# Performance work log

Measured on AMD Instinct MI355X. Metric: run time of the kernel, lower is better.

Reference implementation:

```python
import jax, jax.numpy as jnp
import numpy as np

B, N, M, D, F, H = 8, 512, 512, 512, 512, 8
D_H, F_H = D // H, F // H


def setup_inputs() -> dict:
    key = jax.random.key(0)
    ks = jax.random.split(key, 7)
    X = jax.random.normal(ks[0], (B, N, D), dtype=jnp.float32)
    V = jax.random.normal(ks[1], (B, M, F), dtype=jnp.float32)
    # learned parameters, init normal(0, 0.02) as in the torch module
    W_Q_1 = 0.02 * jax.random.normal(ks[2], (H, N, D_H, D_H), dtype=jnp.float32)
    W_Q_2 = 0.02 * jax.random.normal(ks[3], (H, N, M, D_H), dtype=jnp.float32)
    W_V = 0.02 * jax.random.normal(ks[4], (H, F_H, F_H), dtype=jnp.float32)
    O_w = 0.02 * jax.random.normal(ks[5], (F, F), dtype=jnp.float32)
    O_b = jnp.zeros((F,), dtype=jnp.float32)
    return {"X": X, "V": V, "W_Q_1": W_Q_1, "W_Q_2": W_Q_2,
            "W_V": W_V, "O_w": O_w, "O_b": O_b}


def reference(X, V, W_Q_1, W_Q_2, W_V, O_w, O_b):
    b, n, d = X.shape
    _, m, f = V.shape
    Xh = X.reshape(b, n, H, d // H)      # [B,N,H,D_H]
    Vh = V.reshape(b, m, H, f // H)      # [B,M,H,F_H]
    # 'hndd' repeats d within one operand -> diagonal of W_Q_1's last two dims
    # (faithful to torch.einsum semantics): per-position per-channel scale.
    Q_1 = jnp.einsum('bnhd,hndd->bhnd', Xh, W_Q_1)
    Q_1 = jax.nn.gelu(Q_1, approximate=False)  # torch nn.GELU default = exact erf
    Q_2 = jnp.einsum('bhnd,hnmd->bhnm', Q_1, W_Q_2)  # synthesized attention logits
    A = jax.nn.softmax(Q_2, axis=3)                  # softmax over M
    # 'hff' likewise takes the diagonal of W_V -> per-head channel scale fused
    # with the attention-weighted value aggregation.
    Y = jnp.einsum('bhnm,bmhf,hff->bnhf', A, Vh, W_V)
    Y = Y.reshape(b, n, f)
    return Y @ O_w.T + O_b
```

## Files before the change

### kernel.cpp

```cpp
#include <hip/hip_runtime.h>
#include <cstdint>

#define B_ 8
#define N_ 512
#define M_ 512
#define D_ 512
#define F_ 512
#define H_ 8
#define DH_ 64
#define FH_ 64

typedef __attribute__((ext_vector_type(8))) short bf16x8;
typedef __attribute__((ext_vector_type(4))) float f32x4;
typedef __attribute__((ext_vector_type(8))) unsigned short u16x8;

__device__ __forceinline__ unsigned short f2bf(float x) {
    unsigned u = __float_as_uint(x);
    return (unsigned short)((u + 0x7fffu + ((u >> 16) & 1u)) >> 16);
}
__device__ __forceinline__ float bf2f(unsigned short b) {
    return __uint_as_float(((unsigned)b) << 16);
}

__device__ __forceinline__ f32x4 ntload4(const float* p) {
    return __builtin_nontemporal_load((const f32x4*)p);
}
__device__ __forceinline__ float ntload1(const float* p) {
    return __builtin_nontemporal_load(p);
}

template <int CTRL>
__device__ __forceinline__ float dpp_add(float x) {
    int y = __builtin_amdgcn_update_dpp(0, __float_as_int(x), CTRL, 0xf, 0xf, true);
    return x + __int_as_float(y);
}

__global__ __launch_bounds__(256, 4) void syn_k_attn(const float* __restrict__ X,
                                                     const float* __restrict__ W1,
                                                     const float* __restrict__ W2,
                                                     unsigned short* __restrict__ Ahi,
                                                     unsigned short* __restrict__ Alo) {
    int hn = blockIdx.x;
    int h = hn >> 9, n = hn & 511;
    int t = threadIdx.x;
    int wave = t >> 6, lane = t & 63;
    __shared__ float q1s[8 * 68];
    __shared__ float logits[8 * 520];

    {
        int d = t & 63;
        int b0 = t >> 6;
        float w = ntload1(W1 + (size_t)hn * (DH_ * DH_) + d * (DH_ + 1));
        #pragma unroll
        for (int i = 0; i < 2; ++i) {
            int bi = b0 + i * 4;
            float x = X[((size_t)(bi * N_ + n)) * D_ + h * DH_ + d];
            float v = x * w;
            q1s[bi * 68 + d] = 0.5f * v * (1.0f + erff(v * 0.70710678118654752440f));
        }
    }
    __syncthreads();

    int mr = lane >> 3, c = lane & 7;
    float4 qa[8], qb[8];
    #pragma unroll
    for (int b = 0; b < 8; ++b) {
        qa[b] = *(const float4*)&q1s[b * 68 + c * 8];
        qb[b] = *(const float4*)&q1s[b * 68 + c * 8 + 4];
    }

    const float* w2 = W2 + (size_t)hn * ((size_t)M_ * DH_);
    #pragma unroll 4
    for (int g = 0; g < 16; ++g) {
        int m = (wave + g * 4) * 8 + mr;
        const float* wr = w2 + (size_t)m * DH_ + c * 8;
        f32x4 wa = ntload4(wr);
        f32x4 wb = ntload4(wr + 4);
        float acc[8];
        #pragma unroll
        for (int b = 0; b < 8; ++b) {
            float a0 = wa.x * qa[b].x + wa.y * qa[b].y + wa.z * qa[b].z + wa.w * qa[b].w
                     + wb.x * qb[b].x + wb.y * qb[b].y + wb.z * qb[b].z + wb.w * qb[b].w;
            a0 = dpp_add<0xB1>(a0);
            a0 = dpp_add<0x4E>(a0);
            a0 = dpp_add<0x124>(a0);
            acc[b] = a0;
        }
        float lo = c == 0 ? acc[0] : c == 1 ? acc[1] : c == 2 ? acc[2] : acc[3];
        float hi = c == 0 ? acc[4] : c == 1 ? acc[5] : c == 2 ? acc[6] : acc[7];
        if (c < 4) {
            logits[c * 520 + m] = lo;
            logits[(c + 4) * 520 + m] = hi;
        }
    }
    __syncthreads();

    for (int bb = wave; bb < 8; bb += 4) {
        const float* lrow = &logits[bb * 520 + lane * 8];
        float4 va = *(const float4*)lrow;
        float4 vb = *(const float4*)(lrow + 4);
        float v[8] = {va.x, va.y, va.z, va.w, vb.x, vb.y, vb.z, vb.w};
        float mx = v[0];
        #pragma unroll
        for (int i = 1; i < 8; ++i) mx = fmaxf(mx, v[i]);
        #pragma unroll
        for (int s = 1; s < 64; s <<= 1) mx = fmaxf(mx, __shfl_xor(mx, s));
        float e[8]; float sum = 0.f;
        #pragma unroll
        for (int i = 0; i < 8; ++i) { e[i] = expf(v[i] - mx); sum += e[i]; }
        #pragma unroll
        for (int s = 1; s < 64; s <<= 1) sum += __shfl_xor(sum, s);
        float inv = 1.0f / sum;
        unsigned short hb[8], lb[8];
        #pragma unroll
        for (int i = 0; i < 8; ++i) {
            float y = e[i] * inv;
            hb[i] = f2bf(y);
            lb[i] = f2bf(y - bf2f(hb[i]));
        }
        size_t base = ((size_t)(bb * H_ + h) * N_ + n) * M_ + lane * 8;
        *(u16x8*)(Ahi + base) = *(u16x8*)hb;
        *(u16x8*)(Alo + base) = *(u16x8*)lb;
    }
}

__global__ __launch_bounds__(256) void syn_k_splitw(const float* __restrict__ Ow,
                                                    unsigned short* __restrict__ Whi,
                                                    unsigned short* __restrict__ Wlo) {
    int i = (blockIdx.x * 256 + threadIdx.x) * 4;
    float4 v = *(const float4*)(Ow + i);
    float vv[4] = {v.x, v.y, v.z, v.w};
    unsigned short hb[4], lb[4];
    #pragma unroll
    for (int j = 0; j < 4; ++j) {
        hb[j] = f2bf(vv[j]);
        lb[j] = f2bf(vv[j] - bf2f(hb[j]));
    }
    uint2 hv, lv;
    hv.x = (unsigned)hb[0] | ((unsigned)hb[1] << 16);
    hv.y = (unsigned)hb[2] | ((unsigned)hb[3] << 16);
    lv.x = (unsigned)lb[0] | ((unsigned)lb[1] << 16);
    lv.y = (unsigned)lb[2] | ((unsigned)lb[3] << 16);
    *(uint2*)(Whi + i) = hv;
    *(uint2*)(Wlo + i) = lv;
}

__global__ __launch_bounds__(256) void syn_k_splitv(const float* __restrict__ V,
                                                    unsigned short* __restrict__ Vthi,
                                                    unsigned short* __restrict__ Vtlo) {
    int bh = blockIdx.x;
    int b = bh >> 3, h = bh & 7;
    int t = threadIdx.x;
    __shared__ float lds[64 * 68];
    for (int m0 = 0; m0 < M_; m0 += 64) {
        int m = t >> 2, fo = (t & 3) * 16;
        const float* src = V + ((size_t)(b * M_ + m0 + m)) * F_ + h * FH_ + fo;
        #pragma unroll
        for (int i = 0; i < 4; ++i)
            *(float4*)&lds[m * 68 + fo + i * 4] = *(const float4*)(src + i * 4);
        __syncthreads();
        int f = t >> 2, mo = (t & 3) * 16;
        unsigned short hb[16], lb[16];
        #pragma unroll
        for (int i = 0; i < 16; ++i) {
            float x = lds[(mo + i) * 68 + f];
            hb[i] = f2bf(x);
            lb[i] = f2bf(x - bf2f(hb[i]));
        }
        size_t base = ((size_t)(bh * 64 + f)) * 512 + m0 + mo;
        *(u16x8*)(Vthi + base) = *(u16x8*)hb;
        *(u16x8*)(Vthi + base + 8) = *(u16x8*)&hb[8];
        *(u16x8*)(Vtlo + base) = *(u16x8*)lb;
        *(u16x8*)(Vtlo + base + 8) = *(u16x8*)&lb[8];
        __syncthreads();
    }
}

__global__ __launch_bounds__(256) void syn_k_pv_mfma(const unsigned short* __restrict__ Ahi,
                                                     const unsigned short* __restrict__ Alo,
                                                     const unsigned short* __restrict__ Vthi,
                                                     const unsigned short* __restrict__ Vtlo,
                                                     const float* __restrict__ WV,
                                                     unsigned short* __restrict__ Yhi,
                                                     unsigned short* __restrict__ Ylo) {
    int bh = blockIdx.y;
    int b = bh >> 3, h = bh & 7;
    int n0 = blockIdx.x * 32;
    int t = threadIdx.x;
    int lane = t & 63, wave = t >> 6;
    int wr = wave >> 1, wc = wave & 1;
    __shared__ __align__(16) unsigned short Alh[32 * 64], All[32 * 64];
    __shared__ __align__(16) unsigned short Blh[64 * 64], Bll[64 * 64];
    f32x4 acc[2];
    acc[0] = (f32x4){0.f, 0.f, 0.f, 0.f};
    acc[1] = (f32x4){0.f, 0.f, 0.f, 0.f};

    int srow = t >> 3, skg = t & 7;
    int sslot = skg ^ (srow & 7);
    const unsigned short* Ahb = Ahi + ((size_t)bh * N_ + n0) * M_;
    const unsigned short* Alb = Alo + ((size_t)bh * N_ + n0) * M_;
    const unsigned short* Vhb = Vthi + ((size_t)bh * 64) * 512;
    const unsigned short* Vlb = Vtlo + ((size_t)bh * 64) * 512;

    u16x8 rAh, rAl, rBh0, rBl0, rBh1, rBl1;
    {
        size_t aoff = (size_t)srow * M_ + skg * 8;
        rAh = *(const u16x8*)(Ahb + aoff);
        rAl = *(const u16x8*)(Alb + aoff);
        size_t v0 = (size_t)srow * 512 + skg * 8;
        size_t v1 = (size_t)(srow + 32) * 512 + skg * 8;
        rBh0 = *(const u16x8*)(Vhb + v0);
        rBl0 = *(const u16x8*)(Vlb + v0);
        rBh1 = *(const u16x8*)(Vhb + v1);
        rBl1 = *(const u16x8*)(Vlb + v1);
    }

    #pragma unroll 1
    for (int mb = 0; mb < 8; ++mb) {
        *(u16x8*)&Alh[srow * 64 + sslot * 8] = rAh;
        *(u16x8*)&All[srow * 64 + sslot * 8] = rAl;
        *(u16x8*)&Blh[srow * 64 + sslot * 8] = rBh0;
        *(u16x8*)&Bll[srow * 64 + sslot * 8] = rBl0;
        *(u16x8*)&Blh[(srow + 32) * 64 + sslot * 8] = rBh1;
        *(u16x8*)&Bll[(srow + 32) * 64 + sslot * 8] = rBl1;
        __syncthreads();
        if (mb < 7) {
            int m0 = (mb + 1) * 64;
            size_t aoff = (size_t)srow * M_ + m0 + skg * 8;
            rAh = *(const u16x8*)(Ahb + aoff);
            rAl = *(const u16x8*)(Alb + aoff);
            size_t v0 = (size_t)srow * 512 + m0 + skg * 8;
            size_t v1 = (size_t)(srow + 32) * 512 + m0 + skg * 8;
            rBh0 = *(const u16x8*)(Vhb + v0);
            rBl0 = *(const u16x8*)(Vlb + v0);
            rBh1 = *(const u16x8*)(Vhb + v1);
            rBl1 = *(const u16x8*)(Vlb + v1);
        }
        #pragma unroll
        for (int mg = 0; mg < 2; ++mg) {
            int kslot = (mg * 4 + (lane >> 4)) ^ (lane & 7);
            int arow = wr * 16 + (lane & 15);
            bf16x8 afh = *(const bf16x8*)&Alh[arow * 64 + kslot * 8];
            bf16x8 afl = *(const bf16x8*)&All[arow * 64 + kslot * 8];
            bf16x8 bfh[2], bfl[2];
            #pragma unroll
            for (int j = 0; j < 2; ++j) {
                int brow = wc * 32 + j * 16 + (lane & 15);
                bfh[j] = *(const bf16x8*)&Blh[brow * 64 + kslot * 8];
                bfl[j] = *(const bf16x8*)&Bll[brow * 64 + kslot * 8];
            }
            #pragma unroll
            for (int j = 0; j < 2; ++j) {
                acc[j] = __builtin_amdgcn_mfma_f32_16x16x32_bf16(afh, bfh[j], acc[j], 0, 0, 0);
                acc[j] = __builtin_amdgcn_mfma_f32_16x16x32_bf16(afh, bfl[j], acc[j], 0, 0, 0);
                acc[j] = __builtin_amdgcn_mfma_f32_16x16x32_bf16(afl, bfh[j], acc[j], 0, 0, 0);
            }
        }
        __syncthreads();
    }

    int crow = n0 + wr * 16 + (lane >> 4) * 4;
    int ccol = wc * 32 + (lane & 15);
    #pragma unroll
    for (int j = 0; j < 2; ++j) {
        int f = ccol + j * 16;
        float s = WV[(size_t)h * (FH_ * FH_) + f * (FH_ + 1)];
        #pragma unroll
        for (int r = 0; r < 4; ++r) {
            int row = crow + r;
            float y = acc[j][r] * s;
            unsigned short hb = f2bf(y);
            unsigned short lb = f2bf(y - bf2f(hb));
            size_t base = ((size_t)(b * N_ + row)) * F_ + h * FH_ + f;
            Yhi[base] = hb;
            Ylo[base] = lb;
        }
    }
}

__global__ __launch_bounds__(256) void syn_k_out_mfma(const unsigned short* __restrict__ Yhi,
                                                      const unsigned short* __restrict__ Ylo,
                                                      const unsigned short* __restrict__ Whi,
                                                      const unsigned short* __restrict__ Wlo,
                                                      const float* __restrict__ Ob,
                                                      float* __restrict__ out) {
    int r0 = blockIdx.x * 64;
    int f0 = blockIdx.y * 64;
    int t = threadIdx.x;
    int lane = t & 63, wave = t >> 6;
    int wr = wave >> 1, wc = wave & 1;
    __shared__ __align__(16) unsigned short Alh[64 * 64], All[64 * 64];
    __shared__ __align__(16) unsigned short Blh[64 * 64], Bll[64 * 64];
    f32x4 acc[2][2];
    #pragma unroll
    for (int i = 0; i < 2; ++i)
        #pragma unroll
        for (int j = 0; j < 2; ++j) acc[i][j] = (f32x4){0.f, 0.f, 0.f, 0.f};

    int srow = t >> 3, skg = t & 7;
    int sslot = skg ^ (srow & 7);

    #pragma unroll 1
    for (int kb = 0; kb < 512; kb += 64) {
        #pragma unroll
        for (int rr = 0; rr < 2; ++rr) {
            int row = srow + rr * 32;
            size_t ya = (size_t)(r0 + row) * 512 + kb + skg * 8;
            size_t wa = (size_t)(f0 + row) * 512 + kb + skg * 8;
            *(u16x8*)&Alh[row * 64 + sslot * 8] = *(const u16x8*)(Yhi + ya);
            *(u16x8*)&All[row * 64 + sslot * 8] = *(const u16x8*)(Ylo + ya);
            *(u16x8*)&Blh[row * 64 + sslot * 8] = *(const u16x8*)(Whi + wa);
            *(u16x8*)&Bll[row * 64 + sslot * 8] = *(const u16x8*)(Wlo + wa);
        }
        __syncthreads();
        #pragma unroll
        for (int mg = 0; mg < 2; ++mg) {
            int kslot = (mg * 4 + (lane >> 4)) ^ (lane & 7);
            bf16x8 afh[2], afl[2], bfh[2], bfl[2];
            #pragma unroll
            for (int q = 0; q < 2; ++q) {
                int arow = wr * 32 + q * 16 + (lane & 15);
                afh[q] = *(const bf16x8*)&Alh[arow * 64 + kslot * 8];
                afl[q] = *(const bf16x8*)&All[arow * 64 + kslot * 8];
                int brow = wc * 32 + q * 16 + (lane & 15);
                bfh[q] = *(const bf16x8*)&Blh[brow * 64 + kslot * 8];
                bfl[q] = *(const bf16x8*)&Bll[brow * 64 + kslot * 8];
            }
            #pragma unroll
            for (int i = 0; i < 2; ++i)
                #pragma unroll
                for (int j = 0; j < 2; ++j) {
                    acc[i][j] = __builtin_amdgcn_mfma_f32_16x16x32_bf16(afh[i], bfh[j], acc[i][j], 0, 0, 0);
                    acc[i][j] = __builtin_amdgcn_mfma_f32_16x16x32_bf16(afh[i], bfl[j], acc[i][j], 0, 0, 0);
                    acc[i][j] = __builtin_amdgcn_mfma_f32_16x16x32_bf16(afl[i], bfh[j], acc[i][j], 0, 0, 0);
                }
        }
        __syncthreads();
    }

    int crow = r0 + wr * 32 + (lane >> 4) * 4;
    int ccol = f0 + wc * 32 + (lane & 15);
    float ob0 = Ob[ccol], ob1 = Ob[ccol + 16];
    #pragma unroll
    for (int i = 0; i < 2; ++i)
        #pragma unroll
        for (int j = 0; j < 2; ++j) {
            float obv = (j == 0) ? ob0 : ob1;
            #pragma unroll
            for (int r = 0; r < 4; ++r) {
                int row = crow + i * 16 + r;
                out[(size_t)row * F_ + ccol + j * 16] = acc[i][j][r] + obv;
            }
        }
}

extern "C" void kernel_launch(void* const* d_in, const int* in_sizes, int n_in,
                              void* d_out, int out_size, void* d_ws, size_t ws_size,
                              hipStream_t stream) {
    const float* X  = (const float*)d_in[0];
    const float* V  = (const float*)d_in[1];
    const float* W1 = (const float*)d_in[2];
    const float* W2 = (const float*)d_in[3];
    const float* WV = (const float*)d_in[4];
    const float* Ow = (const float*)d_in[5];
    const float* Ob = (const float*)d_in[6];
    float* out = (float*)d_out;

    unsigned short* Ahi = (unsigned short*)d_ws;
    unsigned short* Alo = Ahi + (size_t)B_ * H_ * N_ * M_;
    unsigned short* Yhi = Alo + (size_t)B_ * H_ * N_ * M_;
    unsigned short* Ylo = Yhi + (size_t)B_ * N_ * F_;
    unsigned short* Whi = Ylo + (size_t)B_ * N_ * F_;
    unsigned short* Wlo = Whi + (size_t)F_ * F_;
    unsigned short* Vthi = Wlo + (size_t)F_ * F_;
    unsigned short* Vtlo = Vthi + (size_t)B_ * H_ * FH_ * M_;

    syn_k_splitw<<<(F_ * F_) / (256 * 4), 256, 0, stream>>>(Ow, Whi, Wlo);
    syn_k_splitv<<<B_ * H_, 256, 0, stream>>>(V, Vthi, Vtlo);
    syn_k_attn<<<H_ * N_, 256, 0, stream>>>(X, W1, W2, Ahi, Alo);
    syn_k_pv_mfma<<<dim3(N_ / 32, B_ * H_), 256, 0, stream>>>(Ahi, Alo, Vthi, Vtlo, WV, Yhi, Ylo);
    syn_k_out_mfma<<<dim3((B_ * N_) / 64, F_ / 64), 256, 0, stream>>>(Yhi, Ylo, Whi, Wlo, Ob, out);
}
```

Baseline: 183.2 us.

## Load MFMA fragments directly from global memory in PV kernel, dropping LDS staging

The PV kernel no longer stages A and V tiles through swizzled shared memory with barriers. Each wave now loads its bf16x8 MFMA operands straight from global memory and walks the M dimension in 32-wide steps, unrolled by 4. Launch bounds now request 4 blocks per CU. This removes LDS traffic and __syncthreads, but V rows are fetched redundantly by the waves sharing them, relying on the cache for reuse, and there is no explicit prefetch to hide global latency.

```diff
diff --git a/kernel.cpp b/kernel.cpp
--- a/kernel.cpp
+++ b/kernel.cpp
@@ -176,91 +176,51 @@
     }
 }
 
-__global__ __launch_bounds__(256) void syn_k_pv_mfma(const unsigned short* __restrict__ Ahi,
-                                                     const unsigned short* __restrict__ Alo,
-                                                     const unsigned short* __restrict__ Vthi,
-                                                     const unsigned short* __restrict__ Vtlo,
-                                                     const float* __restrict__ WV,
-                                                     unsigned short* __restrict__ Yhi,
-                                                     unsigned short* __restrict__ Ylo) {
+__global__ __launch_bounds__(256, 4) void syn_k_pv_mfma(const unsigned short* __restrict__ Ahi,
+                                                        const unsigned short* __restrict__ Alo,
+                                                        const unsigned short* __restrict__ Vthi,
+                                                        const unsigned short* __restrict__ Vtlo,
+                                                        const float* __restrict__ WV,
+                                                        unsigned short* __restrict__ Yhi,
+                                                        unsigned short* __restrict__ Ylo) {
     int bh = blockIdx.y;
     int b = bh >> 3, h = bh & 7;
     int n0 = blockIdx.x * 32;
     int t = threadIdx.x;
     int lane = t & 63, wave = t >> 6;
     int wr = wave >> 1, wc = wave & 1;
-    __shared__ __align__(16) unsigned short Alh[32 * 64], All[32 * 64];
-    __shared__ __align__(16) unsigned short Blh[64 * 64], Bll[64 * 64];
-    f32x4 acc[2];
-    acc[0] = (f32x4){0.f, 0.f, 0.f, 0.f};
-    acc[1] = (f32x4){0.f, 0.f, 0.f, 0.f};
-
-    int srow = t >> 3, skg = t & 7;
-    int sslot = skg ^ (srow & 7);
-    const unsigned short* Ahb = Ahi + ((size_t)bh * N_ + n0) * M_;
-    const unsigned short* Alb = Alo + ((size_t)bh * N_ + n0) * M_;
-    const unsigned short* Vhb = Vthi + ((size_t)bh * 64) * 512;
-    const unsigned short* Vlb = Vtlo + ((size_t)bh * 64) * 512;
-
-    u16x8 rAh, rAl, rBh0, rBl0, rBh1, rBl1;
-    {
-        size_t aoff = (size_t)srow * M_ + skg * 8;
-        rAh = *(const u16x8*)(Ahb + aoff);
-        rAl = *(const u16x8*)(Alb + aoff);
-        size_t v0 = (size_t)srow * 512 + skg * 8;
-        size_t v1 = (size_t)(srow + 32) * 512 + skg * 8;
-        rBh0 = *(const u16x8*)(Vhb + v0);
-        rBl0 = *(const u16x8*)(Vlb + v0);
-        rBh1 = *(const u16x8*)(Vhb + v1);
-        rBl1 = *(const u16x8*)(Vlb + v1);
-    }
-
-    #pragma unroll 1
-    for (int mb = 0; mb < 8; ++mb) {
-        *(u16x8*)&Alh[srow * 64 + sslot * 8] = rAh;
-        *(u16x8*)&All[srow * 64 + sslot * 8] = rAl;
-        *(u16x8*)&Blh[srow * 64 + sslot * 8] = rBh0;
-        *(u16x8*)&Bll[srow * 64 + sslot * 8] = rBl0;
-        *(u16x8*)&Blh[(srow + 32) * 64 + sslot * 8] = rBh1;
-        *(u16x8*)&Bll[(srow + 32) * 64 + sslot * 8] = rBl1;
-        __syncthreads();
-        if (mb < 7) {
-            int m0 = (mb + 1) * 64;
-            size_t aoff = (size_t)srow * M_ + m0 + skg * 8;
-            rAh = *(const u16x8*)(Ahb + aoff);
-            rAl = *(const u16x8*)(Alb + aoff);
-            size_t v0 = (size_t)srow * 512 + m0 + skg * 8;
-            size_t v1 = (size_t)(srow + 32) * 512 + m0 + skg * 8;
-            rBh0 = *(const u16x8*)(Vhb + v0);
-            rBl0 = *(const u16x8*)(Vlb + v0);
-            rBh1 = *(const u16x8*)(Vhb + v1);
-            rBl1 = *(const u16x8*)(Vlb + v1);
-        }
-        #pragma unroll
-        for (int mg = 0; mg < 2; ++mg) {
-            int kslot = (mg * 4 + (lane >> 4)) ^ (lane & 7);
-            int arow = wr * 16 + (lane & 15);
-            bf16x8 afh = *(const bf16x8*)&Alh[arow * 64 + kslot * 8];
-            bf16x8 afl = *(const bf16x8*)&All[arow * 64 + kslot * 8];
-            bf16x8 bfh[2], bfl[2];
-            #pragma unroll
-            for (int j = 0; j < 2; ++j) {
-                int brow = wc * 32 + j * 16 + (lane & 15);
-                bfh[j] = *(const bf16x8*)&Blh[brow * 64 + kslot * 8];
-                bfl[j] = *(const bf16x8*)&Bll[brow * 64 + kslot * 8];
-            }
-            #pragma unroll
-            for (int j = 0; j < 2; ++j) {
-                acc[j] = __builtin_amdgcn_mfma_f32_16x16x32_bf16(afh, bfh[j], acc[j], 0, 0, 0);
-                acc[j] = __builtin_amdgcn_mfma_f32_16x16x32_bf16(afh, bfl[j], acc[j], 0, 0, 0);
-                acc[j] = __builtin_amdgcn_mfma_f32_16x16x32_bf16(afl, bfh[j], acc[j], 0, 0, 0);
-            }
-        }
-        __syncthreads();
+    int row16 = lane & 15, kg = lane >> 4;
+
+    const unsigned short* Ah = Ahi + ((size_t)(bh * N_ + n0 + wr * 16 + row16)) * M_ + kg * 8;
+    const unsigned short* Al = Alo + ((size_t)(bh * N_ + n0 + wr * 16 + row16)) * M_ + kg * 8;
+    const unsigned short* Vh0 = Vthi + ((size_t)(bh * 64 + wc * 32 + row16)) * 512 + kg * 8;
+    const unsigned short* Vl0 = Vtlo + ((size_t)(bh * 64 + wc * 32 + row16)) * 512 + kg * 8;
+    const unsigned short* Vh1 = Vh0 + 16 * 512;
+    const unsigned short* Vl1 = Vl0 + 16 * 512;
+
+    f32x4 acc0 = (f32x4){0.f, 0.f, 0.f, 0.f};
+    f32x4 acc1 = (f32x4){0.f, 0.f, 0.f, 0.f};
+
+    #pragma unroll 4
+    for (int s = 0; s < 16; ++s) {
+        int mo = s * 32;
+        bf16x8 ah  = *(const bf16x8*)(Ah + mo);
+        bf16x8 al  = *(const bf16x8*)(Al + mo);
+        bf16x8 vh0 = *(const bf16x8*)(Vh0 + mo);
+        bf16x8 vl0 = *(const bf16x8*)(Vl0 + mo);
+        bf16x8 vh1 = *(const bf16x8*)(Vh1 + mo);
+        bf16x8 vl1 = *(const bf16x8*)(Vl1 + mo);
+        acc0 = __builtin_amdgcn_mfma_f32_16x16x32_bf16(ah, vh0, acc0, 0, 0, 0);
+        acc0 = __builtin_amdgcn_mfma_f32_16x16x32_bf16(ah, vl0, acc0, 0, 0, 0);
+        acc0 = __builtin_amdgcn_mfma_f32_16x16x32_bf16(al, vh0, acc0, 0, 0, 0);
+        acc1 = __builtin_amdgcn_mfma_f32_16x16x32_bf16(ah, vh1, acc1, 0, 0, 0);
+        acc1 = __builtin_amdgcn_mfma_f32_16x16x32_bf16(ah, vl1, acc1, 0, 0, 0);
+        acc1 = __builtin_amdgcn_mfma_f32_16x16x32_bf16(al, vh1, acc1, 0, 0, 0);
     }
 
     int crow = n0 + wr * 16 + (lane >> 4) * 4;
     int ccol = wc * 32 + (lane & 15);
+    f32x4 accs[2] = {acc0, acc1};
     #pragma unroll
     for (int j = 0; j < 2; ++j) {
         int f = ccol + j * 16;
@@ -268,7 +228,7 @@
         #pragma unroll
         for (int r = 0; r < 4; ++r) {
             int row = crow + r;
-            float y = acc[j][r] * s;
+            float y = accs[j][r] * s;
             unsigned short hb = f2bf(y);
             unsigned short lb = f2bf(y - bf2f(hb));
             size_t base = ((size_t)(b * N_ + row)) * F_ + h * FH_ + f;
```

After: 207.5 us. 1.13x slower.
